# Optimization experiments

Measured on AMD Instinct MI355X. Metric: run time of the kernel, lower is better.

Reference implementation:

```python
import jax, jax.numpy as jnp
import numpy as np

N_NODES = 200000
N_EDGES = 200000
X_SIZE = 256
H_SIZE = 256


def setup_inputs() -> dict:
    key = jax.random.key(0)
    ks = jax.random.split(key, 8)
    s = 1.0 / np.sqrt(H_SIZE)
    return {
        "x": jax.random.normal(ks[0], (N_NODES, X_SIZE), jnp.float32),
        "h": jax.random.normal(ks[1], (N_NODES, H_SIZE), jnp.float32),
        "c": jax.random.normal(ks[2], (N_NODES, H_SIZE), jnp.float32),
        "W_iou": jax.random.normal(ks[3], (3 * H_SIZE, X_SIZE), jnp.float32) * s,
        "U_iou": jax.random.normal(ks[4], (3 * H_SIZE, H_SIZE), jnp.float32) * s,
        "b_iou": jnp.zeros((1, 3 * H_SIZE), jnp.float32),
        "U_f_w": jax.random.normal(ks[5], (H_SIZE, H_SIZE), jnp.float32) * s,
        "U_f_b": jnp.zeros((H_SIZE,), jnp.float32),
        "edge_src": jax.random.randint(ks[6], (N_EDGES,), 0, N_NODES, jnp.int32),
        "edge_dst": jax.random.randint(ks[7], (N_EDGES,), 0, N_NODES, jnp.int32),
    }


def reference(x, h, c, W_iou, U_iou, b_iou, U_f_w, U_f_b, edge_src, edge_dst):
    n = x.shape[0]
    # --- message + reduce (DGL mailbox flattened to edge list) ---
    h_child = h[edge_src]                                   # [E, H] gather
    c_child = c[edge_src]                                   # [E, H]
    f = jax.nn.sigmoid(h_child @ U_f_w.T + U_f_b)           # per-child forget gate
    h_tild = jax.ops.segment_sum(h_child, edge_dst, num_segments=n)      # sum_j h_j
    c_agg = jax.ops.segment_sum(f * c_child, edge_dst, num_segments=n)   # sum_j f_j*c_j
    # --- node iou: W_iou(x) (node data) + U_iou(h_tild) from reduce ---
    iou = x @ W_iou.T + h_tild @ U_iou.T + b_iou            # [N, 3H]
    # --- apply_node_func ---
    i, o, u = jnp.split(iou, 3, axis=1)
    i = jax.nn.sigmoid(i)
    o = jax.nn.sigmoid(o)
    u = jnp.tanh(u)
    c_new = i * u + c_agg
    h_new = o * jnp.tanh(c_new)
    return h_new, c_new
```

## Files before the change

### kernel.cpp

```cpp
#include <hip/hip_runtime.h>

#define NN 200000
#define NE 200000
#define HD 256

typedef __attribute__((ext_vector_type(8))) short short8;
typedef __attribute__((ext_vector_type(4))) short short4v;
typedef __attribute__((ext_vector_type(4))) float f32x4;

static __device__ __forceinline__ unsigned short f2bf(float f) {
  unsigned u = __float_as_uint(f);
  u = (u + 0x7FFFu + ((u >> 16) & 1u)) >> 16;
  return (unsigned short)u;
}
static __device__ __forceinline__ float bf2f(unsigned short u) {
  return __uint_as_float(((unsigned)u) << 16);
}
static __device__ __forceinline__ float sigmoidf_(float x) {
  return 1.0f / (1.0f + __expf(-x));
}
static __device__ __forceinline__ float tanhf_(float x) {
  return 2.0f / (1.0f + __expf(-2.0f * x)) - 1.0f;
}
static __device__ __forceinline__ void atomAddF(float* p, float v) {
  __hip_atomic_fetch_add(p, v, __ATOMIC_RELAXED, __HIP_MEMORY_SCOPE_AGENT);
}
static __device__ __forceinline__ int atomAddI(int* p, int v) {
  return __hip_atomic_fetch_add(p, v, __ATOMIC_RELAXED, __HIP_MEMORY_SCOPE_AGENT);
}

#define OFF_WFB    0u
#define OFF_WIOU   131072u
#define OFF_UIOU   524288u
#define OFF_BPERM  917504u
#define OFF_ROWPTR 920576u
#define OFF_NEXT   1720832u
#define OFF_SLOT   2520832u
#define OFF_PSRC   3320832u
#define OFF_BSUM   4120832u
#define OFF_FC     4121856u
#define WS_NEED    106521856ull

__global__ __launch_bounds__(256) void prep_kernel(
    const float* __restrict__ Ufw, const float* __restrict__ Wiou,
    const float* __restrict__ Uiou, const float* __restrict__ biou,
    unsigned short* __restrict__ Wfb, unsigned short* __restrict__ Wioub,
    unsigned short* __restrict__ Uioub, float* __restrict__ bperm) {
  int idx = blockIdx.x * 256 + threadIdx.x;
  if (idx < 65536) {
    Wfb[idx] = f2bf(Ufw[idx]);
  } else if (idx < 262144) {
    int i2 = idx - 65536;
    int rp = i2 >> 8, k = i2 & 255;
    int T = rp >> 4, cc = rp & 15;
    int g = T % 3, tj = T / 3;
    Wioub[i2] = f2bf(Wiou[(g * 256 + tj * 16 + cc) * 256 + k]);
  } else if (idx < 458752) {
    int i2 = idx - 262144;
    int rp = i2 >> 8, k = i2 & 255;
    int T = rp >> 4, cc = rp & 15;
    int g = T % 3, tj = T / 3;
    Uioub[i2] = f2bf(Uiou[(g * 256 + tj * 16 + cc) * 256 + k]);
  } else if (idx < 459520) {
    int j2 = idx - 458752;
    int T = j2 >> 4, cc = j2 & 15;
    int g = T % 3, tj = T / 3;
    bperm[j2] = biou[g * 256 + tj * 16 + cc];
  }
}

__global__ __launch_bounds__(256) void hist_kernel(const int* __restrict__ edst,
                                                   int* __restrict__ cnt) {
  int e = blockIdx.x * 256 + threadIdx.x;
  if (e < NE) atomAddI(&cnt[edst[e]], 1);
}

__global__ __launch_bounds__(256) void scan_part(const int* __restrict__ cnt,
                                                 int* __restrict__ rp,
                                                 int* __restrict__ bsum) {
  __shared__ int sd[256];
  int t = threadIdx.x;
  int base = blockIdx.x * 1024 + t * 4;
  int v0 = (base + 0 < NN) ? cnt[base + 0] : 0;
  int v1 = (base + 1 < NN) ? cnt[base + 1] : 0;
  int v2 = (base + 2 < NN) ? cnt[base + 2] : 0;
  int v3 = (base + 3 < NN) ? cnt[base + 3] : 0;
  int s = v0 + v1 + v2 + v3;
  sd[t] = s;
  __syncthreads();
  for (int off = 1; off < 256; off <<= 1) {
    int add = (t >= off) ? sd[t - off] : 0;
    __syncthreads();
    sd[t] += add;
    __syncthreads();
  }
  int run = sd[t] - s;
  if (base + 0 < NN) rp[base + 0] = run; run += v0;
  if (base + 1 < NN) rp[base + 1] = run; run += v1;
  if (base + 2 < NN) rp[base + 2] = run; run += v2;
  if (base + 3 < NN) rp[base + 3] = run;
  if (t == 255) bsum[blockIdx.x] = sd[255];
}

__global__ __launch_bounds__(256) void scan_top(int* __restrict__ bsum,
                                                int* __restrict__ rp, int nb) {
  __shared__ int sd[256];
  int t = threadIdx.x;
  int v = (t < nb) ? bsum[t] : 0;
  sd[t] = v;
  __syncthreads();
  for (int off = 1; off < 256; off <<= 1) {
    int add = (t >= off) ? sd[t - off] : 0;
    __syncthreads();
    sd[t] += add;
    __syncthreads();
  }
  bsum[t] = sd[t] - v;
  if (t == 0) rp[NN] = NE;
}

__global__ __launch_bounds__(256) void scan_add(int* __restrict__ rp,
                                                const int* __restrict__ bsum,
                                                int* __restrict__ nxt) {
  int t = threadIdx.x;
  int base = blockIdx.x * 1024 + t * 4;
  int off = bsum[blockIdx.x];
#pragma unroll
  for (int j = 0; j < 4; ++j) {
    int i = base + j;
    if (i < NN) {
      int val = rp[i] + off;
      rp[i] = val;
      nxt[i] = val;
    }
  }
}

__global__ __launch_bounds__(256) void scatter_kernel(
    const int* __restrict__ esrc, const int* __restrict__ edst,
    int* __restrict__ nxt, int* __restrict__ slotArr, int* __restrict__ psrc) {
  int e = blockIdx.x * 256 + threadIdx.x;
  if (e < NE) {
    int d = edst[e];
    int pos = atomAddI(&nxt[d], 1);
    slotArr[e] = pos;
    psrc[pos] = esrc[e];
  }
}

#define F_AS 72
#define F_BS 72

__global__ __launch_bounds__(256) void edge_fc_kernel(
    const float* __restrict__ h, const float* __restrict__ c,
    const unsigned short* __restrict__ Wfb, const float* __restrict__ Ufb,
    const int* __restrict__ esrc, const int* __restrict__ slotArr,
    unsigned short* __restrict__ fcb) {
  __shared__ __align__(16) unsigned short Als[64 * F_AS];
  __shared__ __align__(16) unsigned short Bls[256 * F_BS];
  __shared__ int srcl[64], slotl[64];

  const int tid = threadIdx.x;
  const int e0 = blockIdx.x * 64;
  if (tid < 64) { srcl[tid] = esrc[e0 + tid]; slotl[tid] = slotArr[e0 + tid]; }
  __syncthreads();

  const int lane = tid & 63;
  const int wv = tid >> 6;
  const int wm = wv >> 1, wn = wv & 1;
  const int cbase = lane & 15;
  const int kg = lane >> 4;

  f32x4 acc[2][8];
#pragma unroll
  for (int i = 0; i < 2; ++i)
#pragma unroll
    for (int j = 0; j < 8; ++j) acc[i][j] = {0.f, 0.f, 0.f, 0.f};

  const int arow = tid >> 2;
  const int acg = tid & 3;
  const float* hrow = h + (size_t)srcl[arow] * HD;

  for (int kc = 0; kc < 4; ++kc) {
    const int k0 = kc * 64;
    const float4* s4 = (const float4*)(hrow + k0 + acg * 16);
    float4 q0 = s4[0], q1 = s4[1], q2 = s4[2], q3 = s4[3];
    short8 p0, p1;
    p0[0] = f2bf(q0.x); p0[1] = f2bf(q0.y); p0[2] = f2bf(q0.z); p0[3] = f2bf(q0.w);
    p0[4] = f2bf(q1.x); p0[5] = f2bf(q1.y); p0[6] = f2bf(q1.z); p0[7] = f2bf(q1.w);
    p1[0] = f2bf(q2.x); p1[1] = f2bf(q2.y); p1[2] = f2bf(q2.z); p1[3] = f2bf(q2.w);
    p1[4] = f2bf(q3.x); p1[5] = f2bf(q3.y); p1[6] = f2bf(q3.z); p1[7] = f2bf(q3.w);
    short8* ap = (short8*)&Als[arow * F_AS + acg * 16];
    ap[0] = p0; ap[1] = p1;
#pragma unroll
    for (int i = 0; i < 8; ++i) {
      int f = tid + 256 * i;
      int row = f >> 3, ch = f & 7;
      short8 vb = *(const short8*)(Wfb + row * 256 + k0 + ch * 8);
      *(short8*)&Bls[row * F_BS + ch * 8] = vb;
    }
    __syncthreads();
#pragma unroll
    for (int ks = 0; ks < 2; ++ks) {
      short8 a0 = *(const short8*)&Als[(wm * 32 + cbase) * F_AS + ks * 32 + kg * 8];
      short8 a1 = *(const short8*)&Als[(wm * 32 + 16 + cbase) * F_AS + ks * 32 + kg * 8];
#pragma unroll
      for (int nt = 0; nt < 8; ++nt) {
        short8 b = *(const short8*)&Bls[(wn * 128 + nt * 16 + cbase) * F_BS + ks * 32 + kg * 8];
        acc[0][nt] = __builtin_amdgcn_mfma_f32_16x16x32_bf16(a0, b, acc[0][nt], 0, 0, 0);
        acc[1][nt] = __builtin_amdgcn_mfma_f32_16x16x32_bf16(a1, b, acc[1][nt], 0, 0, 0);
      }
    }
    __syncthreads();
  }
  const int rsub = kg * 4;
#pragma unroll
  for (int nt = 0; nt < 8; ++nt) {
    const int coln = wn * 128 + nt * 16 + cbase;
    const float bias = Ufb[coln];
#pragma unroll
    for (int mt = 0; mt < 2; ++mt) {
#pragma unroll
      for (int j = 0; j < 4; ++j) {
        const int el = wm * 32 + mt * 16 + rsub + j;
        const float fg = sigmoidf_(acc[mt][nt][j] + bias);
        const float cv = c[(size_t)srcl[el] * HD + coln];
        fcb[(size_t)slotl[el] * HD + coln] = f2bf(fg * cv);
      }
    }
  }
}

#define HLS_SWZ(row, byteoff) (((row) * 512 + (byteoff)) ^ (((row) & 7) << 4))

__global__ __launch_bounds__(512) void iou_fused_kernel(
    const float* __restrict__ x, const float* __restrict__ h,
    const unsigned short* __restrict__ Wioub, const unsigned short* __restrict__ Uioub,
    const float* __restrict__ bperm, const int* __restrict__ rp,
    const int* __restrict__ psrc, const unsigned short* __restrict__ fcb,
    float* __restrict__ out) {
  __shared__ __align__(16) unsigned short Bls[768 * 40];
  __shared__ __align__(16) unsigned char HlsB[64 * 512];
  __shared__ __align__(4) unsigned short Cls[64 * 258];

  const int tid = threadIdx.x;
  const int r0 = blockIdx.x * 64;

  {
    const int node = tid >> 3;
    const int cg = tid & 7;
    const int n = r0 + node;
    const int s0 = rp[n], s1 = rp[n + 1];
    float4 hs[8], cs[8];
#pragma unroll
    for (int q = 0; q < 8; ++q) { hs[q] = {0.f, 0.f, 0.f, 0.f}; cs[q] = {0.f, 0.f, 0.f, 0.f}; }
    for (int s = s0; s < s1; ++s) {
      const int src = psrc[s];
      const float4* hp = (const float4*)(h + (size_t)src * HD + cg * 32);
#pragma unroll
      for (int q = 0; q < 8; ++q) {
        float4 v = hp[q];
        hs[q].x += v.x; hs[q].y += v.y; hs[q].z += v.z; hs[q].w += v.w;
      }
      const short8* fp = (const short8*)(fcb + (size_t)s * HD + cg * 32);
#pragma unroll
      for (int q = 0; q < 4; ++q) {
        short8 w = fp[q];
        cs[2 * q].x     += bf2f((unsigned short)w[0]);
        cs[2 * q].y     += bf2f((unsigned short)w[1]);
        cs[2 * q].z     += bf2f((unsigned short)w[2]);
        cs[2 * q].w     += bf2f((unsigned short)w[3]);
        cs[2 * q + 1].x += bf2f((unsigned short)w[4]);
        cs[2 * q + 1].y += bf2f((unsigned short)w[5]);
        cs[2 * q + 1].z += bf2f((unsigned short)w[6]);
        cs[2 * q + 1].w += bf2f((unsigned short)w[7]);
      }
    }
#pragma unroll
    for (int q = 0; q < 4; ++q) {
      short8 hp8;
      hp8[0] = f2bf(hs[2 * q].x);     hp8[1] = f2bf(hs[2 * q].y);
      hp8[2] = f2bf(hs[2 * q].z);     hp8[3] = f2bf(hs[2 * q].w);
      hp8[4] = f2bf(hs[2 * q + 1].x); hp8[5] = f2bf(hs[2 * q + 1].y);
      hp8[6] = f2bf(hs[2 * q + 1].z); hp8[7] = f2bf(hs[2 * q + 1].w);
      *(short8*)&HlsB[HLS_SWZ(node, cg * 64 + q * 16)] = hp8;
      unsigned short* cd = &Cls[node * 258 + cg * 32 + q * 8];
      cd[0] = f2bf(cs[2 * q].x);     cd[1] = f2bf(cs[2 * q].y);
      cd[2] = f2bf(cs[2 * q].z);     cd[3] = f2bf(cs[2 * q].w);
      cd[4] = f2bf(cs[2 * q + 1].x); cd[5] = f2bf(cs[2 * q + 1].y);
      cd[6] = f2bf(cs[2 * q + 1].z); cd[7] = f2bf(cs[2 * q + 1].w);
    }
  }
  __syncthreads();

  const int lane = tid & 63;
  const int wv = tid >> 6;
  const int wm = wv >> 2;
  const int wn = wv & 3;
  const int cbase = lane & 15;
  const int kg = lane >> 4;

  f32x4 acc[2][12];
#pragma unroll
  for (int m = 0; m < 2; ++m)
#pragma unroll
    for (int t = 0; t < 12; ++t) acc[m][t] = {0.f, 0.f, 0.f, 0.f};

  for (int pass = 0; pass < 2; ++pass) {
    const unsigned short* Bs = pass ? Uioub : Wioub;
    for (int kc = 0; kc < 8; ++kc) {
      const int k0 = kc * 32;
#pragma unroll
      for (int i = 0; i < 6; ++i) {
        int f = tid + 512 * i;
        int row = f >> 2, ch = f & 3;
        short8 vb = *(const short8*)(Bs + row * 256 + k0 + ch * 8);
        *(short8*)&Bls[row * 40 + ch * 8] = vb;
      }
      short8 a0, a1;
      if (pass == 0) {
        const float4* xp0 = (const float4*)(x + (size_t)(r0 + wm * 32 + cbase) * HD + k0 + kg * 8);
        const float4* xp1 = (const float4*)(x + (size_t)(r0 + wm * 32 + 16 + cbase) * HD + k0 + kg * 8);
        float4 u0 = xp0[0], u1 = xp0[1], u2 = xp1[0], u3 = xp1[1];
        a0[0] = f2bf(u0.x); a0[1] = f2bf(u0.y); a0[2] = f2bf(u0.z); a0[3] = f2bf(u0.w);
        a0[4] = f2bf(u1.x); a0[5] = f2bf(u1.y); a0[6] = f2bf(u1.z); a0[7] = f2bf(u1.w);
        a1[0] = f2bf(u2.x); a1[1] = f2bf(u2.y); a1[2] = f2bf(u2.z); a1[3] = f2bf(u2.w);
        a1[4] = f2bf(u3.x); a1[5] = f2bf(u3.y); a1[6] = f2bf(u3.z); a1[7] = f2bf(u3.w);
      }
      __syncthreads();
      if (pass == 1) {
        a0 = *(const short8*)&HlsB[HLS_SWZ(wm * 32 + cbase, k0 * 2 + kg * 16)];
        a1 = *(const short8*)&HlsB[HLS_SWZ(wm * 32 + 16 + cbase, k0 * 2 + kg * 16)];
      }
#pragma unroll
      for (int tt = 0; tt < 12; ++tt) {
        short8 b = *(const short8*)&Bls[((wn * 12 + tt) * 16 + cbase) * 40 + kg * 8];
        acc[0][tt] = __builtin_amdgcn_mfma_f32_16x16x32_bf16(a0, b, acc[0][tt], 0, 0, 0);
        acc[1][tt] = __builtin_amdgcn_mfma_f32_16x16x32_bf16(a1, b, acc[1][tt], 0, 0, 0);
      }
      __syncthreads();
    }
  }

  const int rsub = kg * 4;
#pragma unroll
  for (int t3 = 0; t3 < 4; ++t3) {
    const int T = wn * 12 + 3 * t3;
    const float bi = bperm[(T + 0) * 16 + cbase];
    const float bo = bperm[(T + 1) * 16 + cbase];
    const float bu = bperm[(T + 2) * 16 + cbase];
    const int j = (wn * 4 + t3) * 16 + cbase;
#pragma unroll
    for (int mf = 0; mf < 2; ++mf) {
#pragma unroll
      for (int jr = 0; jr < 4; ++jr) {
        const int rl = wm * 32 + mf * 16 + rsub + jr;
        const size_t idx = (size_t)(r0 + rl) * HD + j;
        const float iv = sigmoidf_(acc[mf][3 * t3 + 0][jr] + bi);
        const float ov = sigmoidf_(acc[mf][3 * t3 + 1][jr] + bo);
        const float uv = tanhf_(acc[mf][3 * t3 + 2][jr] + bu);
        const float cagg = bf2f(Cls[rl * 258 + j]);
        const float cn = iv * uv + cagg;
        out[idx] = ov * tanhf_(cn);
        out[(size_t)NN * HD + idx] = cn;
      }
    }
  }
}

__global__ __launch_bounds__(256) void edge_kernel(
    const float* __restrict__ h, const float* __restrict__ c,
    const unsigned short* __restrict__ Wfb, const float* __restrict__ Ufb,
    const int* __restrict__ esrc, const int* __restrict__ edst,
    float* h_tild, float* c_agg) {
  __shared__ __align__(16) unsigned short Als[64 * F_AS];
  __shared__ __align__(16) unsigned short Bls[256 * F_BS];
  __shared__ int srcl[64], dstl[64];

  const int tid = threadIdx.x;
  const int e0 = blockIdx.x * 64;
  if (tid < 64) { srcl[tid] = esrc[e0 + tid]; dstl[tid] = edst[e0 + tid]; }
  __syncthreads();

  const int lane = tid & 63;
  const int wv = tid >> 6;
  const int wm = wv >> 1, wn = wv & 1;
  const int cbase = lane & 15;
  const int kg = lane >> 4;

  f32x4 acc[2][8];
#pragma unroll
  for (int i = 0; i < 2; ++i)
#pragma unroll
    for (int j = 0; j < 8; ++j) acc[i][j] = {0.f, 0.f, 0.f, 0.f};

  const int arow = tid >> 2;
  const int acg = tid & 3;
  const float* hrow = h + (size_t)srcl[arow] * HD;
  float* htrow = h_tild + (size_t)dstl[arow] * HD;

  for (int kc = 0; kc < 4; ++kc) {
    const int k0 = kc * 64;
    const float4* s4 = (const float4*)(hrow + k0 + acg * 16);
    float4 q0 = s4[0], q1 = s4[1], q2 = s4[2], q3 = s4[3];
    short8 p0, p1;
    p0[0] = f2bf(q0.x); p0[1] = f2bf(q0.y); p0[2] = f2bf(q0.z); p0[3] = f2bf(q0.w);
    p0[4] = f2bf(q1.x); p0[5] = f2bf(q1.y); p0[6] = f2bf(q1.z); p0[7] = f2bf(q1.w);
    p1[0] = f2bf(q2.x); p1[1] = f2bf(q2.y); p1[2] = f2bf(q2.z); p1[3] = f2bf(q2.w);
    p1[4] = f2bf(q3.x); p1[5] = f2bf(q3.y); p1[6] = f2bf(q3.z); p1[7] = f2bf(q3.w);
    short8* ap = (short8*)&Als[arow * F_AS + acg * 16];
    ap[0] = p0; ap[1] = p1;
    {
      float* hp = htrow + k0 + acg * 16;
      atomAddF(hp + 0, q0.x);  atomAddF(hp + 1, q0.y);
      atomAddF(hp + 2, q0.z);  atomAddF(hp + 3, q0.w);
      atomAddF(hp + 4, q1.x);  atomAddF(hp + 5, q1.y);
      atomAddF(hp + 6, q1.z);  atomAddF(hp + 7, q1.w);
      atomAddF(hp + 8, q2.x);  atomAddF(hp + 9, q2.y);
      atomAddF(hp + 10, q2.z); atomAddF(hp + 11, q2.w);
      atomAddF(hp + 12, q3.x); atomAddF(hp + 13, q3.y);
      atomAddF(hp + 14, q3.z); atomAddF(hp + 15, q3.w);
    }
#pragma unroll
    for (int i = 0; i < 8; ++i) {
      int f = tid + 256 * i;
      int row = f >> 3, ch = f & 7;
      short8 vb = *(const short8*)(Wfb + row * 256 + k0 + ch * 8);
      *(short8*)&Bls[row * F_BS + ch * 8] = vb;
    }
    __syncthreads();
#pragma unroll
    for (int ks = 0; ks < 2; ++ks) {
      short8 a0 = *(const short8*)&Als[(wm * 32 + cbase) * F_AS + ks * 32 + kg * 8];
      short8 a1 = *(const short8*)&Als[(wm * 32 + 16 + cbase) * F_AS + ks * 32 + kg * 8];
#pragma unroll
      for (int nt = 0; nt < 8; ++nt) {
        short8 b = *(const short8*)&Bls[(wn * 128 + nt * 16 + cbase) * F_BS + ks * 32 + kg * 8];
        acc[0][nt] = __builtin_amdgcn_mfma_f32_16x16x32_bf16(a0, b, acc[0][nt], 0, 0, 0);
        acc[1][nt] = __builtin_amdgcn_mfma_f32_16x16x32_bf16(a1, b, acc[1][nt], 0, 0, 0);
      }
    }
    __syncthreads();
  }
  const int rsub = kg * 4;
#pragma unroll
  for (int nt = 0; nt < 8; ++nt) {
    const int coln = wn * 128 + nt * 16 + cbase;
    const float bias = Ufb[coln];
#pragma unroll
    for (int mt = 0; mt < 2; ++mt) {
#pragma unroll
      for (int j = 0; j < 4; ++j) {
        const int el = wm * 32 + mt * 16 + rsub + j;
        const float fg = sigmoidf_(acc[mt][nt][j] + bias);
        const float cv = c[(size_t)srcl[el] * HD + coln];
        atomAddF(c_agg + (size_t)dstl[el] * HD + coln, fg * cv);
      }
    }
  }
}

#define I_AS 40
#define I_BS 40

__global__ __launch_bounds__(256) void iou_kernel(
    const float* __restrict__ x, const unsigned short* __restrict__ Wioub,
    const unsigned short* __restrict__ Uioub, const float* __restrict__ bperm,
    float* out) {
  __shared__ __align__(16) unsigned short Als[32 * I_AS];
  __shared__ __align__(16) unsigned short Bls[768 * I_BS];

  const int tid = threadIdx.x;
  const int lane = tid & 63;
  const int wv = tid >> 6;
  const int wm = wv >> 1, wn = wv & 1;
  const int cbase = lane & 15;
  const int kg = lane >> 4;
  const int r0 = blockIdx.x * 32;

  float* h_tild = out;
  float* c_agg = out + (size_t)NN * HD;

  f32x4 acc[24];
#pragma unroll
  for (int t = 0; t < 24; ++t) acc[t] = {0.f, 0.f, 0.f, 0.f};

  const int arow = tid >> 3;
  const int acg = tid & 7;

  for (int pass = 0; pass < 2; ++pass) {
    const float* As = pass ? h_tild : x;
    const unsigned short* Bs = pass ? Uioub : Wioub;
    for (int kc = 0; kc < 8; ++kc) {
      const int k0 = kc * 32;
      float4 q = *(const float4*)(As + (size_t)(r0 + arow) * HD + k0 + acg * 4);
      short4v p;
      p[0] = f2bf(q.x); p[1] = f2bf(q.y); p[2] = f2bf(q.z); p[3] = f2bf(q.w);
      *(short4v*)&Als[arow * I_AS + acg * 4] = p;
#pragma unroll
      for (int i = 0; i < 12; ++i) {
        int f = tid + 256 * i;
        int row = f >> 2, ch = f & 3;
        short8 vb = *(const short8*)(Bs + row * 256 + k0 + ch * 8);
        *(short8*)&Bls[row * I_BS + ch * 8] = vb;
      }
      __syncthreads();
      short8 a = *(const short8*)&Als[(wm * 16 + cbase) * I_AS + kg * 8];
#pragma unroll
      for (int tt = 0; tt < 24; ++tt) {
        short8 b = *(const short8*)&Bls[((wn * 24 + tt) * 16 + cbase) * I_BS + kg * 8];
        acc[tt] = __builtin_amdgcn_mfma_f32_16x16x32_bf16(a, b, acc[tt], 0, 0, 0);
      }
      __syncthreads();
    }
  }
  const int rsub = kg * 4;
#pragma unroll
  for (int t3 = 0; t3 < 8; ++t3) {
    const int T = wn * 24 + 3 * t3;
    const float bi = bperm[(T + 0) * 16 + cbase];
    const float bo = bperm[(T + 1) * 16 + cbase];
    const float bu = bperm[(T + 2) * 16 + cbase];
    const int j = (wn * 8 + t3) * 16 + cbase;
#pragma unroll
    for (int jr = 0; jr < 4; ++jr) {
      const int r = r0 + wm * 16 + rsub + jr;
      const size_t idx = (size_t)r * HD + j;
      const float iv = sigmoidf_(acc[3 * t3 + 0][jr] + bi);
      const float ov = sigmoidf_(acc[3 * t3 + 1][jr] + bo);
      const float uv = tanhf_(acc[3 * t3 + 2][jr] + bu);
      const float cn = iv * uv + c_agg[idx];
      out[idx] = ov * tanhf_(cn);
      c_agg[idx] = cn;
    }
  }
}

extern "C" void kernel_launch(void* const* d_in, const int* in_sizes, int n_in,
                              void* d_out, int out_size, void* d_ws, size_t ws_size,
                              hipStream_t stream) {
  const float* x    = (const float*)d_in[0];
  const float* h    = (const float*)d_in[1];
  const float* c    = (const float*)d_in[2];
  const float* Wiou = (const float*)d_in[3];
  const float* Uiou = (const float*)d_in[4];
  const float* biou = (const float*)d_in[5];
  const float* Ufw  = (const float*)d_in[6];
  const float* Ufb  = (const float*)d_in[7];
  const int* esrc   = (const int*)d_in[8];
  const int* edst   = (const int*)d_in[9];
  float* out = (float*)d_out;

  char* ws = (char*)d_ws;
  unsigned short* Wfb   = (unsigned short*)(ws + OFF_WFB);
  unsigned short* Wioub = (unsigned short*)(ws + OFF_WIOU);
  unsigned short* Uioub = (unsigned short*)(ws + OFF_UIOU);
  float* bperm          = (float*)(ws + OFF_BPERM);

  if (ws_size >= WS_NEED) {
    int* rpp  = (int*)(ws + OFF_ROWPTR);
    int* nxt  = (int*)(ws + OFF_NEXT);
    int* slot = (int*)(ws + OFF_SLOT);
    int* psrc = (int*)(ws + OFF_PSRC);
    int* bsum = (int*)(ws + OFF_BSUM);
    unsigned short* fcb = (unsigned short*)(ws + OFF_FC);

    hipMemsetAsync(nxt, 0, (size_t)NN * sizeof(int), stream);
    prep_kernel<<<1795, 256, 0, stream>>>(Ufw, Wiou, Uiou, biou, Wfb, Wioub, Uioub, bperm);
    hist_kernel<<<(NE + 255) / 256, 256, 0, stream>>>(edst, nxt);
    scan_part<<<(NN + 1023) / 1024, 256, 0, stream>>>(nxt, rpp, bsum);
    scan_top<<<1, 256, 0, stream>>>(bsum, rpp, (NN + 1023) / 1024);
    scan_add<<<(NN + 1023) / 1024, 256, 0, stream>>>(rpp, bsum, nxt);
    scatter_kernel<<<(NE + 255) / 256, 256, 0, stream>>>(esrc, edst, nxt, slot, psrc);
    edge_fc_kernel<<<NE / 64, 256, 0, stream>>>(h, c, Wfb, Ufb, esrc, slot, fcb);
    iou_fused_kernel<<<NN / 64, 512, 0, stream>>>(x, h, Wioub, Uioub, bperm, rpp, psrc, fcb, out);
  } else {
    hipMemsetAsync(d_out, 0, (size_t)out_size * sizeof(float), stream);
    prep_kernel<<<1795, 256, 0, stream>>>(Ufw, Wiou, Uiou, biou, Wfb, Wioub, Uioub, bperm);
    edge_kernel<<<NE / 64, 256, 0, stream>>>(h, c, Wfb, Ufb, esrc, edst,
                                             out, out + (size_t)NN * HD);
    iou_kernel<<<NN / 32, 256, 0, stream>>>(x, Wioub, Uioub, bperm, out);
  }
}
```

Before: 795.8 us.

## Split neighbor gather from IOU GEMM and stream pre-swizzled weights via direct LDS loads

The fused IOU kernel is split in two. A standalone gather kernel writes c_agg in fp32 to the output buffer and stores the bf16 h_tild sum in place of the first fcb slot of each node. The GEMM kernel then reads h_tild rows straight from global memory, using a zero page for nodes with no children. The weights are pre-packed into one MFMA-fragment-ordered buffer covering both x and h_tild K-chunks and copied with global_load_lds, which shrinks LDS use so more blocks can fit per CU (launch_bounds 512,4). The cost is an extra kernel launch, an fp32 c_agg round trip through global memory, and a small hazard from overwriting fcb in place.

Result: slower. 849.5 us (+6.8%).

```diff
diff --git a/kernel.cpp b/kernel.cpp
--- a/kernel.cpp
+++ b/kernel.cpp
@@ -29,19 +29,58 @@
   return __hip_atomic_fetch_add(p, v, __ATOMIC_RELAXED, __HIP_MEMORY_SCOPE_AGENT);
 }
 
+#if __has_builtin(__builtin_amdgcn_global_load_lds)
+#define HAVE_GLDS 1
+static __device__ __forceinline__ void gload_lds16(const void* g, void* l) {
+  __builtin_amdgcn_global_load_lds(
+      (const __attribute__((address_space(1))) void*)g,
+      (__attribute__((address_space(3))) void*)l, 16, 0, 0);
+}
+#endif
+
 #define OFF_WFB    0u
-#define OFF_WIOU   131072u
-#define OFF_UIOU   524288u
+#define OFF_BP     131072u
 #define OFF_BPERM  917504u
 #define OFF_ROWPTR 920576u
 #define OFF_NEXT   1720832u
 #define OFF_SLOT   2520832u
 #define OFF_PSRC   3320832u
 #define OFF_BSUM   4120832u
-#define OFF_FC     4121856u
-#define WS_NEED    106521856ull
+#define OFF_ZERO   4121856u
+#define OFF_FC     4122880u
+#define WS_NEED    106522880ull
+#define WS_NEED_FB 1048576ull
 
 __global__ __launch_bounds__(256) void prep_kernel(
+    const float* __restrict__ Ufw, const float* __restrict__ Wiou,
+    const float* __restrict__ Uiou, const float* __restrict__ biou,
+    unsigned short* __restrict__ Wfb, unsigned short* __restrict__ Bp,
+    float* __restrict__ bperm) {
+  int idx = blockIdx.x * 256 + threadIdx.x;
+  if (idx < 65536) {
+    Wfb[idx] = f2bf(Ufw[idx]);
+  } else if (idx < 458752) {
+    int o = idx - 65536;
+    int kc = o / 24576;
+    int rem = o - kc * 24576;
+    int tt = rem / 512;
+    int rem2 = rem - tt * 512;
+    int ln = rem2 >> 3, e = rem2 & 7;
+    int cc = ln & 15, kgp = ln >> 4;
+    int kk = kc * 32 + kgp * 8 + e;
+    int g = tt % 3, tj = tt / 3;
+    int orow = g * 256 + tj * 16 + cc;
+    float v = (kk < 256) ? Wiou[orow * 256 + kk] : Uiou[orow * 256 + (kk - 256)];
+    Bp[o] = f2bf(v);
+  } else if (idx < 459520) {
+    int j2 = idx - 458752;
+    int T = j2 >> 4, cc = j2 & 15;
+    int g = T % 3, tj = T / 3;
+    bperm[j2] = biou[g * 256 + tj * 16 + cc];
+  }
+}
+
+__global__ __launch_bounds__(256) void prep_fb_kernel(
     const float* __restrict__ Ufw, const float* __restrict__ Wiou,
     const float* __restrict__ Uiou, const float* __restrict__ biou,
     unsigned short* __restrict__ Wfb, unsigned short* __restrict__ Wioub,
@@ -231,74 +270,77 @@
   }
 }
 
-#define HLS_SWZ(row, byteoff) (((row) * 512 + (byteoff)) ^ (((row) & 7) << 4))
-
-__global__ __launch_bounds__(512) void iou_fused_kernel(
-    const float* __restrict__ x, const float* __restrict__ h,
-    const unsigned short* __restrict__ Wioub, const unsigned short* __restrict__ Uioub,
+__global__ __launch_bounds__(256) void gather_kernel(
+    const float* __restrict__ h, const int* __restrict__ rp,
+    const int* __restrict__ psrc, unsigned short* __restrict__ fcb,
+    float* __restrict__ cagg) {
+  const int tid = threadIdx.x;
+  const int node = blockIdx.x * 32 + (tid >> 3);
+  const int cg = tid & 7;
+  const int s0 = rp[node], s1 = rp[node + 1];
+
+  float hs[32], cs[32];
+#pragma unroll
+  for (int q = 0; q < 32; ++q) { hs[q] = 0.f; cs[q] = 0.f; }
+
+  for (int s = s0; s < s1; ++s) {
+    const int src = psrc[s];
+    const float4* hp = (const float4*)(h + (size_t)src * HD + cg * 32);
+    const short8* fp = (const short8*)(fcb + (size_t)s * HD + cg * 32);
+#pragma unroll
+    for (int q = 0; q < 8; ++q) {
+      float4 v = hp[q];
+      hs[4 * q + 0] += v.x; hs[4 * q + 1] += v.y;
+      hs[4 * q + 2] += v.z; hs[4 * q + 3] += v.w;
+    }
+#pragma unroll
+    for (int q = 0; q < 4; ++q) {
+      short8 w = fp[q];
+#pragma unroll
+      for (int e = 0; e < 8; ++e) cs[8 * q + e] += bf2f((unsigned short)w[e]);
+    }
+  }
+  float4* cp = (float4*)(cagg + (size_t)node * HD + cg * 32);
+#pragma unroll
+  for (int q = 0; q < 8; ++q) {
+    float4 v = {cs[4 * q + 0], cs[4 * q + 1], cs[4 * q + 2], cs[4 * q + 3]};
+    cp[q] = v;
+  }
+  if (s1 > s0) {
+    short8* hd = (short8*)(fcb + (size_t)s0 * HD + cg * 32);
+#pragma unroll
+    for (int q = 0; q < 4; ++q) {
+      short8 p;
+#pragma unroll
+      for (int e = 0; e < 8; ++e) p[e] = f2bf(hs[8 * q + e]);
+      hd[q] = p;
+    }
+  }
+}
+
+__global__ __launch_bounds__(512, 4) void iou_gemm_kernel(
+    const float* __restrict__ x, const unsigned short* __restrict__ Bp,
     const float* __restrict__ bperm, const int* __restrict__ rp,
-    const int* __restrict__ psrc, const unsigned short* __restrict__ fcb,
+    const unsigned short* __restrict__ fcb, const char* __restrict__ zpage,
     float* __restrict__ out) {
-  __shared__ __align__(16) unsigned short Bls[768 * 40];
-  __shared__ __align__(16) unsigned char HlsB[64 * 512];
-  __shared__ __align__(4) unsigned short Cls[64 * 258];
+  __shared__ __align__(16) unsigned short Bls[48 * 512];
 
   const int tid = threadIdx.x;
-  const int r0 = blockIdx.x * 64;
-
-  {
-    const int node = tid >> 3;
-    const int cg = tid & 7;
-    const int n = r0 + node;
-    const int s0 = rp[n], s1 = rp[n + 1];
-    float4 hs[8], cs[8];
-#pragma unroll
-    for (int q = 0; q < 8; ++q) { hs[q] = {0.f, 0.f, 0.f, 0.f}; cs[q] = {0.f, 0.f, 0.f, 0.f}; }
-    for (int s = s0; s < s1; ++s) {
-      const int src = psrc[s];
-      const float4* hp = (const float4*)(h + (size_t)src * HD + cg * 32);
-#pragma unroll
-      for (int q = 0; q < 8; ++q) {
-        float4 v = hp[q];
-        hs[q].x += v.x; hs[q].y += v.y; hs[q].z += v.z; hs[q].w += v.w;
-      }
-      const short8* fp = (const short8*)(fcb + (size_t)s * HD + cg * 32);
-#pragma unroll
-      for (int q = 0; q < 4; ++q) {
-        short8 w = fp[q];
-        cs[2 * q].x     += bf2f((unsigned short)w[0]);
-        cs[2 * q].y     += bf2f((unsigned short)w[1]);
-        cs[2 * q].z     += bf2f((unsigned short)w[2]);
-        cs[2 * q].w     += bf2f((unsigned short)w[3]);
-        cs[2 * q + 1].x += bf2f((unsigned short)w[4]);
-        cs[2 * q + 1].y += bf2f((unsigned short)w[5]);
-        cs[2 * q + 1].z += bf2f((unsigned short)w[6]);
-        cs[2 * q + 1].w += bf2f((unsigned short)w[7]);
-      }
-    }
-#pragma unroll
-    for (int q = 0; q < 4; ++q) {
-      short8 hp8;
-      hp8[0] = f2bf(hs[2 * q].x);     hp8[1] = f2bf(hs[2 * q].y);
-      hp8[2] = f2bf(hs[2 * q].z);     hp8[3] = f2bf(hs[2 * q].w);
-      hp8[4] = f2bf(hs[2 * q + 1].x); hp8[5] = f2bf(hs[2 * q + 1].y);
-      hp8[6] = f2bf(hs[2 * q + 1].z); hp8[7] = f2bf(hs[2 * q + 1].w);
-      *(short8*)&HlsB[HLS_SWZ(node, cg * 64 + q * 16)] = hp8;
-      unsigned short* cd = &Cls[node * 258 + cg * 32 + q * 8];
-      cd[0] = f2bf(cs[2 * q].x);     cd[1] = f2bf(cs[2 * q].y);
-      cd[2] = f2bf(cs[2 * q].z);     cd[3] = f2bf(cs[2 * q].w);
-      cd[4] = f2bf(cs[2 * q + 1].x); cd[5] = f2bf(cs[2 * q + 1].y);
-      cd[6] = f2bf(cs[2 * q + 1].z); cd[7] = f2bf(cs[2 * q + 1].w);
-    }
-  }
-  __syncthreads();
-
   const int lane = tid & 63;
   const int wv = tid >> 6;
-  const int wm = wv >> 2;
-  const int wn = wv & 3;
+  const int wm = wv >> 2, wn = wv & 3;
   const int cbase = lane & 15;
   const int kg = lane >> 4;
+  const int r0 = blockIdx.x * 64;
+  const int row0 = r0 + wm * 32 + cbase;
+  const int row1 = row0 + 16;
+
+  const int sa0 = rp[row0], ea0 = rp[row0 + 1];
+  const int sa1 = rp[row1], ea1 = rp[row1 + 1];
+  const char* pH0 = (ea0 > sa0) ? (const char*)(fcb + (size_t)sa0 * HD) : zpage;
+  const char* pH1 = (ea1 > sa1) ? (const char*)(fcb + (size_t)sa1 * HD) : zpage;
+  const float* pX0 = x + (size_t)row0 * HD;
+  const float* pX1 = x + (size_t)row1 * HD;
 
   f32x4 acc[2][12];
 #pragma unroll
@@ -306,43 +348,47 @@
 #pragma unroll
     for (int t = 0; t < 12; ++t) acc[m][t] = {0.f, 0.f, 0.f, 0.f};
 
-  for (int pass = 0; pass < 2; ++pass) {
-    const unsigned short* Bs = pass ? Uioub : Wioub;
-    for (int kc = 0; kc < 8; ++kc) {
-      const int k0 = kc * 32;
-#pragma unroll
-      for (int i = 0; i < 6; ++i) {
-        int f = tid + 512 * i;
-        int row = f >> 2, ch = f & 3;
-        short8 vb = *(const short8*)(Bs + row * 256 + k0 + ch * 8);
-        *(short8*)&Bls[row * 40 + ch * 8] = vb;
-      }
-      short8 a0, a1;
-      if (pass == 0) {
-        const float4* xp0 = (const float4*)(x + (size_t)(r0 + wm * 32 + cbase) * HD + k0 + kg * 8);
-        const float4* xp1 = (const float4*)(x + (size_t)(r0 + wm * 32 + 16 + cbase) * HD + k0 + kg * 8);
-        float4 u0 = xp0[0], u1 = xp0[1], u2 = xp1[0], u3 = xp1[1];
-        a0[0] = f2bf(u0.x); a0[1] = f2bf(u0.y); a0[2] = f2bf(u0.z); a0[3] = f2bf(u0.w);
-        a0[4] = f2bf(u1.x); a0[5] = f2bf(u1.y); a0[6] = f2bf(u1.z); a0[7] = f2bf(u1.w);
-        a1[0] = f2bf(u2.x); a1[1] = f2bf(u2.y); a1[2] = f2bf(u2.z); a1[3] = f2bf(u2.w);
-        a1[4] = f2bf(u3.x); a1[5] = f2bf(u3.y); a1[6] = f2bf(u3.z); a1[7] = f2bf(u3.w);
-      }
-      __syncthreads();
-      if (pass == 1) {
-        a0 = *(const short8*)&HlsB[HLS_SWZ(wm * 32 + cbase, k0 * 2 + kg * 16)];
-        a1 = *(const short8*)&HlsB[HLS_SWZ(wm * 32 + 16 + cbase, k0 * 2 + kg * 16)];
-      }
-#pragma unroll
-      for (int tt = 0; tt < 12; ++tt) {
-        short8 b = *(const short8*)&Bls[((wn * 12 + tt) * 16 + cbase) * 40 + kg * 8];
-        acc[0][tt] = __builtin_amdgcn_mfma_f32_16x16x32_bf16(a0, b, acc[0][tt], 0, 0, 0);
-        acc[1][tt] = __builtin_amdgcn_mfma_f32_16x16x32_bf16(a1, b, acc[1][tt], 0, 0, 0);
-      }
-      __syncthreads();
-    }
-  }
-
-  const int rsub = kg * 4;
+  for (int kc = 0; kc < 16; ++kc) {
+    const char* gB = (const char*)Bp + kc * 49152 + wv * 1024 + lane * 16;
+    char* lB = (char*)Bls + wv * 1024;
+#ifdef HAVE_GLDS
+#pragma unroll
+    for (int i = 0; i < 6; ++i) gload_lds16(gB + i * 8192, lB + i * 8192);
+#else
+#pragma unroll
+    for (int i = 0; i < 6; ++i) {
+      short8 v = *(const short8*)(gB + i * 8192);
+      *(short8*)(lB + lane * 16 + i * 8192) = v;
+    }
+#endif
+    short8 a0, a1;
+    const int k0 = (kc & 7) * 32;
+    if (kc < 8) {
+      float4 u0 = *(const float4*)(pX0 + k0 + kg * 8);
+      float4 u1 = *(const float4*)(pX0 + k0 + kg * 8 + 4);
+      float4 u2 = *(const float4*)(pX1 + k0 + kg * 8);
+      float4 u3 = *(const float4*)(pX1 + k0 + kg * 8 + 4);
+      a0[0] = f2bf(u0.x); a0[1] = f2bf(u0.y); a0[2] = f2bf(u0.z); a0[3] = f2bf(u0.w);
+      a0[4] = f2bf(u1.x); a0[5] = f2bf(u1.y); a0[6] = f2bf(u1.z); a0[7] = f2bf(u1.w);
+      a1[0] = f2bf(u2.x); a1[1] = f2bf(u2.y); a1[2] = f2bf(u2.z); a1[3] = f2bf(u2.w);
+      a1[4] = f2bf(u3.x); a1[5] = f2bf(u3.y); a1[6] = f2bf(u3.z); a1[7] = f2bf(u3.w);
+    } else {
+      a0 = *(const short8*)(pH0 + k0 * 2 + kg * 16);
+      a1 = *(const short8*)(pH1 + k0 * 2 + kg * 16);
+    }
+    __syncthreads();
+    const char* bbase = (const char*)Bls + (wn * 12) * 1024 + lane * 16;
+#pragma unroll
+    for (int tt = 0; tt < 12; ++tt) {
+      short8 b = *(const short8*)(bbase + tt * 1024);
+      acc[0][tt] = __builtin_amdgcn_mfma_f32_16x16x32_bf16(a0, b, acc[0][tt], 0, 0, 0);
+      acc[1][tt] = __builtin_amdgcn_mfma_f32_16x16x32_bf16(a1, b, acc[1][tt], 0, 0, 0);
+    }
+    __syncthreads();
+  }
+
+  float* outc = out + (size_t)NN * HD;
+  const int rbase = wm * 32 + kg * 4;
 #pragma unroll
   for (int t3 = 0; t3 < 4; ++t3) {
     const int T = wn * 12 + 3 * t3;
@@ -354,15 +400,14 @@
     for (int mf = 0; mf < 2; ++mf) {
 #pragma unroll
       for (int jr = 0; jr < 4; ++jr) {
-        const int rl = wm * 32 + mf * 16 + rsub + jr;
+        const int rl = rbase + mf * 16 + jr;
         const size_t idx = (size_t)(r0 + rl) * HD + j;
         const float iv = sigmoidf_(acc[mf][3 * t3 + 0][jr] + bi);
         const float ov = sigmoidf_(acc[mf][3 * t3 + 1][jr] + bo);
         const float uv = tanhf_(acc[mf][3 * t3 + 2][jr] + bu);
-        const float cagg = bf2f(Cls[rl * 258 + j]);
-        const float cn = iv * uv + cagg;
+        const float cn = iv * uv + outc[idx];
         out[idx] = ov * tanhf_(cn);
-        out[(size_t)NN * HD + idx] = cn;
+        outc[idx] = cn;
       }
     }
   }
@@ -553,8 +598,7 @@
 
   char* ws = (char*)d_ws;
   unsigned short* Wfb   = (unsigned short*)(ws + OFF_WFB);
-  unsigned short* Wioub = (unsigned short*)(ws + OFF_WIOU);
-  unsigned short* Uioub = (unsigned short*)(ws + OFF_UIOU);
+  unsigned short* Bp    = (unsigned short*)(ws + OFF_BP);
   float* bperm          = (float*)(ws + OFF_BPERM);
 
   if (ws_size >= WS_NEED) {
@@ -563,20 +607,25 @@
     int* slot = (int*)(ws + OFF_SLOT);
     int* psrc = (int*)(ws + OFF_PSRC);
     int* bsum = (int*)(ws + OFF_BSUM);
+    char* zpage = ws + OFF_ZERO;
     unsigned short* fcb = (unsigned short*)(ws + OFF_FC);
 
     hipMemsetAsync(nxt, 0, (size_t)NN * sizeof(int), stream);
-    prep_kernel<<<1795, 256, 0, stream>>>(Ufw, Wiou, Uiou, biou, Wfb, Wioub, Uioub, bperm);
+    hipMemsetAsync(zpage, 0, 1024, stream);
+    prep_kernel<<<1795, 256, 0, stream>>>(Ufw, Wiou, Uiou, biou, Wfb, Bp, bperm);
     hist_kernel<<<(NE + 255) / 256, 256, 0, stream>>>(edst, nxt);
     scan_part<<<(NN + 1023) / 1024, 256, 0, stream>>>(nxt, rpp, bsum);
     scan_top<<<1, 256, 0, stream>>>(bsum, rpp, (NN + 1023) / 1024);
     scan_add<<<(NN + 1023) / 1024, 256, 0, stream>>>(rpp, bsum, nxt);
     scatter_kernel<<<(NE + 255) / 256, 256, 0, stream>>>(esrc, edst, nxt, slot, psrc);
     edge_fc_kernel<<<NE / 64, 256, 0, stream>>>(h, c, Wfb, Ufb, esrc, slot, fcb);
-    iou_fused_kernel<<<NN / 64, 512, 0, stream>>>(x, h, Wioub, Uioub, bperm, rpp, psrc, fcb, out);
+    gather_kernel<<<NN / 32, 256, 0, stream>>>(h, rpp, psrc, fcb, out + (size_t)NN * HD);
+    iou_gemm_kernel<<<NN / 64, 512, 0, stream>>>(x, Bp, bperm, rpp, fcb, zpage, out);
   } else {
+    unsigned short* Wioub = (unsigned short*)(ws + OFF_BP);
+    unsigned short* Uioub = (unsigned short*)(ws + OFF_BP + 393216);
     hipMemsetAsync(d_out, 0, (size_t)out_size * sizeof(float), stream);
-    prep_kernel<<<1795, 256, 0, stream>>>(Ufw, Wiou, Uiou, biou, Wfb, Wioub, Uioub, bperm);
+    prep_fb_kernel<<<1795, 256, 0, stream>>>(Ufw, Wiou, Uiou, biou, Wfb, Wioub, Uioub, bperm);
     edge_kernel<<<NE / 64, 256, 0, stream>>>(h, c, Wfb, Ufb, esrc, edst,
                                              out, out + (size_t)NN * HD);
     iou_kernel<<<NN / 32, 256, 0, stream>>>(x, Wioub, Uioub, bperm, out);
```

## Pre-swizzle IOU weights into MFMA fragment order and load from global with double buffering

Applied to the files above, without the earlier changes.

The prep kernel now writes the concatenated W_iou/U_iou weights as bf16 in exact per-lane MFMA fragment order, so the fused IOU kernel loads B fragments straight from global (L2-resident) into registers. This removes the shared-memory B tile, its staging copies and both per-chunk __syncthreads. It also double-buffers B and x loads across a single 16-step K loop and asks for 2 blocks per CU. In exchange it uses many more registers (24 short8 plus x buffers) and every wave re-reads the weights from cache instead of sharing one staged tile.

Measured after the change: 1.123 ms. +41.1%, slower.

```diff
diff --git a/kernel.cpp b/kernel.cpp
--- a/kernel.cpp
+++ b/kernel.cpp
@@ -30,18 +30,47 @@
 }
 
 #define OFF_WFB    0u
-#define OFF_WIOU   131072u
-#define OFF_UIOU   524288u
+#define OFF_BP     131072u
 #define OFF_BPERM  917504u
 #define OFF_ROWPTR 920576u
 #define OFF_NEXT   1720832u
 #define OFF_SLOT   2520832u
 #define OFF_PSRC   3320832u
 #define OFF_BSUM   4120832u
-#define OFF_FC     4121856u
-#define WS_NEED    106521856ull
+#define OFF_ZERO   4121856u
+#define OFF_FC     4122880u
+#define WS_NEED    106522880ull
 
 __global__ __launch_bounds__(256) void prep_kernel(
+    const float* __restrict__ Ufw, const float* __restrict__ Wiou,
+    const float* __restrict__ Uiou, const float* __restrict__ biou,
+    unsigned short* __restrict__ Wfb, unsigned short* __restrict__ Bp,
+    float* __restrict__ bperm) {
+  int idx = blockIdx.x * 256 + threadIdx.x;
+  if (idx < 65536) {
+    Wfb[idx] = f2bf(Ufw[idx]);
+  } else if (idx < 458752) {
+    int o = idx - 65536;
+    int kc = o / 24576;
+    int rem = o - kc * 24576;
+    int tt = rem / 512;
+    int rem2 = rem - tt * 512;
+    int ln = rem2 >> 3, e = rem2 & 7;
+    int cc = ln & 15, kgp = ln >> 4;
+    int kk = kc * 32 + kgp * 8 + e;
+    int g = tt % 3, tj = tt / 3;
+    int orow = g * 256 + tj * 16 + cc;
+    float v = (kk < 256) ? Wiou[orow * 256 + kk] : Uiou[orow * 256 + (kk - 256)];
+    Bp[o] = f2bf(v);
+  } else if (idx < 459520) {
+    int j2 = idx - 458752;
+    int T = j2 >> 4, cc = j2 & 15;
+    int g = T % 3, tj = T / 3;
+    bperm[j2] = biou[g * 256 + tj * 16 + cc];
+  }
+}
+
+__global__ __launch_bounds__(256) void prep_fb_kernel(
     const float* __restrict__ Ufw, const float* __restrict__ Wiou,
     const float* __restrict__ Uiou, const float* __restrict__ biou,
     unsigned short* __restrict__ Wfb, unsigned short* __restrict__ Wioub,
@@ -233,13 +262,11 @@
 
 #define HLS_SWZ(row, byteoff) (((row) * 512 + (byteoff)) ^ (((row) & 7) << 4))
 
-__global__ __launch_bounds__(512) void iou_fused_kernel(
+__global__ __launch_bounds__(512, 2) void iou_fused_kernel(
     const float* __restrict__ x, const float* __restrict__ h,
-    const unsigned short* __restrict__ Wioub, const unsigned short* __restrict__ Uioub,
-    const float* __restrict__ bperm, const int* __restrict__ rp,
-    const int* __restrict__ psrc, const unsigned short* __restrict__ fcb,
-    float* __restrict__ out) {
-  __shared__ __align__(16) unsigned short Bls[768 * 40];
+    const unsigned short* __restrict__ Bp, const float* __restrict__ bperm,
+    const int* __restrict__ rp, const int* __restrict__ psrc,
+    const unsigned short* __restrict__ fcb, float* __restrict__ out) {
   __shared__ __align__(16) unsigned char HlsB[64 * 512];
   __shared__ __align__(4) unsigned short Cls[64 * 258];
 
@@ -295,10 +322,13 @@
 
   const int lane = tid & 63;
   const int wv = tid >> 6;
-  const int wm = wv >> 2;
-  const int wn = wv & 3;
+  const int wm = wv >> 2, wn = wv & 3;
   const int cbase = lane & 15;
   const int kg = lane >> 4;
+  const int row0l = wm * 32 + cbase;
+  const float* pX0 = x + (size_t)(r0 + row0l) * HD;
+  const float* pX1 = x + (size_t)(r0 + row0l + 16) * HD;
+  const char* pB = (const char*)Bp + ((size_t)(wn * 12) * 64 + lane) * 16;
 
   f32x4 acc[2][12];
 #pragma unroll
@@ -306,42 +336,51 @@
 #pragma unroll
     for (int t = 0; t < 12; ++t) acc[m][t] = {0.f, 0.f, 0.f, 0.f};
 
-  for (int pass = 0; pass < 2; ++pass) {
-    const unsigned short* Bs = pass ? Uioub : Wioub;
-    for (int kc = 0; kc < 8; ++kc) {
-      const int k0 = kc * 32;
-#pragma unroll
-      for (int i = 0; i < 6; ++i) {
-        int f = tid + 512 * i;
-        int row = f >> 2, ch = f & 3;
-        short8 vb = *(const short8*)(Bs + row * 256 + k0 + ch * 8);
-        *(short8*)&Bls[row * 40 + ch * 8] = vb;
-      }
-      short8 a0, a1;
-      if (pass == 0) {
-        const float4* xp0 = (const float4*)(x + (size_t)(r0 + wm * 32 + cbase) * HD + k0 + kg * 8);
-        const float4* xp1 = (const float4*)(x + (size_t)(r0 + wm * 32 + 16 + cbase) * HD + k0 + kg * 8);
-        float4 u0 = xp0[0], u1 = xp0[1], u2 = xp1[0], u3 = xp1[1];
-        a0[0] = f2bf(u0.x); a0[1] = f2bf(u0.y); a0[2] = f2bf(u0.z); a0[3] = f2bf(u0.w);
-        a0[4] = f2bf(u1.x); a0[5] = f2bf(u1.y); a0[6] = f2bf(u1.z); a0[7] = f2bf(u1.w);
-        a1[0] = f2bf(u2.x); a1[1] = f2bf(u2.y); a1[2] = f2bf(u2.z); a1[3] = f2bf(u2.w);
-        a1[4] = f2bf(u3.x); a1[5] = f2bf(u3.y); a1[6] = f2bf(u3.z); a1[7] = f2bf(u3.w);
-      }
-      __syncthreads();
-      if (pass == 1) {
-        a0 = *(const short8*)&HlsB[HLS_SWZ(wm * 32 + cbase, k0 * 2 + kg * 16)];
-        a1 = *(const short8*)&HlsB[HLS_SWZ(wm * 32 + 16 + cbase, k0 * 2 + kg * 16)];
-      }
-#pragma unroll
-      for (int tt = 0; tt < 12; ++tt) {
-        short8 b = *(const short8*)&Bls[((wn * 12 + tt) * 16 + cbase) * 40 + kg * 8];
-        acc[0][tt] = __builtin_amdgcn_mfma_f32_16x16x32_bf16(a0, b, acc[0][tt], 0, 0, 0);
-        acc[1][tt] = __builtin_amdgcn_mfma_f32_16x16x32_bf16(a1, b, acc[1][tt], 0, 0, 0);
-      }
-      __syncthreads();
-    }
-  }
-
+  short8 Bf[2][12];
+  float4 Xr[2][4];
+
+#pragma unroll
+  for (int t = 0; t < 12; ++t) Bf[0][t] = *(const short8*)(pB + t * 1024);
+  Xr[0][0] = *(const float4*)(pX0 + kg * 8);
+  Xr[0][1] = *(const float4*)(pX0 + kg * 8 + 4);
+  Xr[0][2] = *(const float4*)(pX1 + kg * 8);
+  Xr[0][3] = *(const float4*)(pX1 + kg * 8 + 4);
+
+#pragma unroll
+  for (int kc = 0; kc < 16; ++kc) {
+    const int cur = kc & 1, nxt = cur ^ 1;
+    if (kc < 15) {
+      const char* pBn = pB + (kc + 1) * 49152;
+#pragma unroll
+      for (int t = 0; t < 12; ++t) Bf[nxt][t] = *(const short8*)(pBn + t * 1024);
+      if (kc + 1 < 8) {
+        const int k0n = (kc + 1) * 32;
+        Xr[nxt][0] = *(const float4*)(pX0 + k0n + kg * 8);
+        Xr[nxt][1] = *(const float4*)(pX0 + k0n + kg * 8 + 4);
+        Xr[nxt][2] = *(const float4*)(pX1 + k0n + kg * 8);
+        Xr[nxt][3] = *(const float4*)(pX1 + k0n + kg * 8 + 4);
+      }
+    }
+    short8 a0, a1;
+    if (kc < 8) {
+      float4 u0 = Xr[cur][0], u1 = Xr[cur][1], u2 = Xr[cur][2], u3 = Xr[cur][3];
+      a0[0] = f2bf(u0.x); a0[1] = f2bf(u0.y); a0[2] = f2bf(u0.z); a0[3] = f2bf(u0.w);
+      a0[4] = f2bf(u1.x); a0[5] = f2bf(u1.y); a0[6] = f2bf(u1.z); a0[7] = f2bf(u1.w);
+      a1[0] = f2bf(u2.x); a1[1] = f2bf(u2.y); a1[2] = f2bf(u2.z); a1[3] = f2bf(u2.w);
+      a1[4] = f2bf(u3.x); a1[5] = f2bf(u3.y); a1[6] = f2bf(u3.z); a1[7] = f2bf(u3.w);
+    } else {
+      const int bo = (kc - 8) * 64 + kg * 16;
+      a0 = *(const short8*)&HlsB[HLS_SWZ(row0l, bo)];
+      a1 = *(const short8*)&HlsB[HLS_SWZ(row0l + 16, bo)];
+    }
+#pragma unroll
+    for (int tt = 0; tt < 12; ++tt) {
+      acc[0][tt] = __builtin_amdgcn_mfma_f32_16x16x32_bf16(a0, Bf[cur][tt], acc[0][tt], 0, 0, 0);
+      acc[1][tt] = __builtin_amdgcn_mfma_f32_16x16x32_bf16(a1, Bf[cur][tt], acc[1][tt], 0, 0, 0);
+    }
+  }
+
+  float* outc = out + (size_t)NN * HD;
   const int rsub = kg * 4;
 #pragma unroll
   for (int t3 = 0; t3 < 4; ++t3) {
@@ -362,7 +401,7 @@
         const float cagg = bf2f(Cls[rl * 258 + j]);
         const float cn = iv * uv + cagg;
         out[idx] = ov * tanhf_(cn);
-        out[(size_t)NN * HD + idx] = cn;
+        outc[idx] = cn;
       }
     }
   }
@@ -553,8 +592,7 @@
 
   char* ws = (char*)d_ws;
   unsigned short* Wfb   = (unsigned short*)(ws + OFF_WFB);
-  unsigned short* Wioub = (unsigned short*)(ws + OFF_WIOU);
-  unsigned short* Uioub = (unsigned short*)(ws + OFF_UIOU);
+  unsigned short* Bp    = (unsigned short*)(ws + OFF_BP);
   float* bperm          = (float*)(ws + OFF_BPERM);
 
   if (ws_size >= WS_NEED) {
@@ -565,18 +603,20 @@
     int* bsum = (int*)(ws + OFF_BSUM);
     unsigned short* fcb = (unsigned short*)(ws + OFF_FC);
 
-    hipMemsetAsync(nxt, 0, (size_t)NN * sizeof(int), stream);
-    prep_kernel<<<1795, 256, 0, stream>>>(Ufw, Wiou, Uiou, biou, Wfb, Wioub, Uioub, bperm);
+    (void)hipMemsetAsync(nxt, 0, (size_t)NN * sizeof(int), stream);
+    prep_kernel<<<1795, 256, 0, stream>>>(Ufw, Wiou, Uiou, biou, Wfb, Bp, bperm);
     hist_kernel<<<(NE + 255) / 256, 256, 0, stream>>>(edst, nxt);
     scan_part<<<(NN + 1023) / 1024, 256, 0, stream>>>(nxt, rpp, bsum);
     scan_top<<<1, 256, 0, stream>>>(bsum, rpp, (NN + 1023) / 1024);
     scan_add<<<(NN + 1023) / 1024, 256, 0, stream>>>(rpp, bsum, nxt);
     scatter_kernel<<<(NE + 255) / 256, 256, 0, stream>>>(esrc, edst, nxt, slot, psrc);
     edge_fc_kernel<<<NE / 64, 256, 0, stream>>>(h, c, Wfb, Ufb, esrc, slot, fcb);
-    iou_fused_kernel<<<NN / 64, 512, 0, stream>>>(x, h, Wioub, Uioub, bperm, rpp, psrc, fcb, out);
+    iou_fused_kernel<<<NN / 64, 512, 0, stream>>>(x, h, Bp, bperm, rpp, psrc, fcb, out);
   } else {
-    hipMemsetAsync(d_out, 0, (size_t)out_size * sizeof(float), stream);
-    prep_kernel<<<1795, 256, 0, stream>>>(Ufw, Wiou, Uiou, biou, Wfb, Wioub, Uioub, bperm);
+    unsigned short* Wioub = (unsigned short*)(ws + OFF_BP);
+    unsigned short* Uioub = (unsigned short*)(ws + OFF_BP + 393216);
+    (void)hipMemsetAsync(d_out, 0, (size_t)out_size * sizeof(float), stream);
+    prep_fb_kernel<<<1795, 256, 0, stream>>>(Ufw, Wiou, Uiou, biou, Wfb, Wioub, Uioub, bperm);
     edge_kernel<<<NE / 64, 256, 0, stream>>>(h, c, Wfb, Ufb, esrc, edst,
                                              out, out + (size_t)NN * HD);
     iou_kernel<<<NN / 32, 256, 0, stream>>>(x, Wioub, Uioub, bperm, out);
```
